# Optimization experiments

Measured on AMD Instinct MI355X. Metric: run time of the kernel, lower is better.

Reference implementation:

```python
import jax, jax.numpy as jnp
import numpy as np

EPS = 1e-6

def _conv1x1(x, w, b):
    # x: [b,c,h,w], w: [o,c], b: [o] -> per-pixel matmul
    return jnp.einsum('bchw,oc->bohw', x, w) + b[None, :, None, None]

def setup_inputs() -> dict:
    key = jax.random.key(0)
    ks = jax.random.split(key, 10)
    b, c, h, w = 16, 256, 128, 128
    dec = jax.random.normal(ks[0], (b, c, h, w), jnp.float32)
    enc = jax.random.normal(ks[1], (b, c, h, w), jnp.float32)
    ln_w = jnp.ones((c,), jnp.float32)
    ln_b = jnp.zeros((c,), jnp.float32)
    w0 = jax.random.normal(ks[2], (c, c), jnp.float32) * 0.05
    b0 = jax.random.normal(ks[3], (c,), jnp.float32) * 0.05
    w1 = jax.random.normal(ks[4], (c // 2, c), jnp.float32) * 0.05
    b1 = jax.random.normal(ks[5], (c // 2,), jnp.float32) * 0.05
    w2 = jax.random.normal(ks[6], (c // 4, c // 2), jnp.float32) * 0.05
    b2 = jax.random.normal(ks[7], (c // 4,), jnp.float32) * 0.05
    w3 = jax.random.normal(ks[8], (1, c // 4), jnp.float32) * 0.05
    b3 = jax.random.normal(ks[9], (1,), jnp.float32) * 0.05
    return dict(dec=dec, enc=enc, ln_w=ln_w, ln_b=ln_b, w0=w0, b0=b0,
                w1=w1, b1=b1, w2=w2, b2=b2, w3=w3, b3=b3)

def reference(dec, enc, ln_w, ln_b, w0, b0, w1, b1, w2, b2, w3, b3):
    b, c, h, w = dec.shape
    x = dec + enc
    # LayerNorm2d: normalize over channel dim per pixel (biased var, eps=1e-6)
    mu = jnp.mean(x, axis=1, keepdims=True)
    var = jnp.var(x, axis=1, keepdims=True)
    x = (x - mu) / jnp.sqrt(var + EPS) * ln_w[None, :, None, None] + ln_b[None, :, None, None]
    # in_conv: 1x1 conv + exact GELU
    x = jax.nn.gelu(_conv1x1(x, w0, b0), approximate=False)
    # split: local channels kept, global channels pooled and broadcast back
    local_x = x[:, :c // 2]                                   # [b,c/2,h,w]
    global_x = jnp.mean(x[:, c // 2:], axis=(2, 3), keepdims=True)  # [b,c/2,1,1]
    x = jnp.concatenate([local_x, jnp.broadcast_to(global_x, local_x.shape)], axis=1)
    # mask_pre: nc -> nc/2 -> nc/4 -> 1 with GELUs
    x = jax.nn.gelu(_conv1x1(x, w1, b1), approximate=False)
    x = jax.nn.gelu(_conv1x1(x, w2, b2), approximate=False)
    x = _conv1x1(x, w3, b3)
    return jax.nn.sigmoid(x)
```

## Files before the change

### kernel.cpp

```cpp
#include <hip/hip_runtime.h>
#include <math.h>

typedef float f32x4 __attribute__((ext_vector_type(4)));
typedef short s8v __attribute__((ext_vector_type(8)));

#define LN_EPS 1e-6f

static __device__ __forceinline__ unsigned short f2bf(float f) {
  union { float f; unsigned int u; } v; v.f = f;
  unsigned int r = (v.u + 0x7FFFu + ((v.u >> 16) & 1u)) >> 16;
  return (unsigned short)r;
}
static __device__ __forceinline__ float bf2f(unsigned short b) {
  union { float f; unsigned int u; } v; v.u = ((unsigned int)b) << 16;
  return v.f;
}
static __device__ __forceinline__ float gelu_fast(float x) {
  float t = x * x;
  float u = x * fmaf(t, 0.07135481283f, 1.5957691216f);
  float e = __expf(-u);
  return __fdividef(x, 1.0f + e);
}

__global__ void prep_kernel(const float* __restrict__ w0, const float* __restrict__ w1,
                            const float* __restrict__ w2, const float* __restrict__ lnw,
                            const float* __restrict__ lnb, const float* __restrict__ b0,
                            unsigned short* __restrict__ wt0f, unsigned short* __restrict__ w1f,
                            unsigned short* __restrict__ w2f, float* __restrict__ gacc,
                            float* __restrict__ sfold, float* __restrict__ tfold) {
  int idx = blockIdx.x * blockDim.x + threadIdx.x;
  int stride = gridDim.x * blockDim.x;
  const int N0 = 65536, N1 = 16384, N2 = 8192, N3 = 2048, N4 = 256;
  for (int i = idx; i < N0 + N1 + N2 + N3 + N4; i += stride) {
    if (i < N0) {
      int j = i & 7, l = (i >> 3) & 63, ks = (i >> 9) & 7, n0 = i >> 12;
      int k = ks * 32 + (l >> 4) * 8 + j;
      wt0f[i] = f2bf(w0[(n0 * 16 + (l & 15)) * 256 + k] * lnw[k]);
    } else if (i < N0 + N1) {
      int t = i - N0;
      int j = t & 7, l = (t >> 3) & 63, ks = (t >> 9) & 3, n0 = t >> 11;
      w1f[t] = f2bf(w1[(n0 * 16 + (l & 15)) * 256 + ks * 32 + (l >> 4) * 8 + j]);
    } else if (i < N0 + N1 + N2) {
      int t = i - N0 - N1;
      int j = t & 7, l = (t >> 3) & 63, ks = (t >> 9) & 3, n0 = t >> 11;
      w2f[t] = f2bf(w2[(n0 * 16 + (l & 15)) * 128 + ks * 32 + (l >> 4) * 8 + j]);
    } else if (i < N0 + N1 + N2 + N3) {
      gacc[i - N0 - N1 - N2] = 0.0f;
    } else {
      int n = i - N0 - N1 - N2 - N3;
      float s = 0.f, t = 0.f;
      for (int c = 0; c < 256; ++c) {
        float wv = w0[n * 256 + c];
        s += wv * lnw[c];
        t += wv * lnb[c];
      }
      sfold[n] = s;
      tfold[n] = t + b0[n];
    }
  }
}

__global__ __launch_bounds__(256, 2) void k1_kernel(
    const float* __restrict__ dec, const float* __restrict__ enc,
    const unsigned short* __restrict__ wt0f,
    const float* __restrict__ sfold, const float* __restrict__ tfold,
    unsigned short* __restrict__ yl, float* __restrict__ gacc) {
  __shared__ __align__(16) unsigned char At[64 * 512];
  __shared__ float red[16][16][8];
  __shared__ float alphaL[64], betaL[64];

  const int tid = threadIdx.x, blk = blockIdx.x;
  const int b = blk >> 8;
  const int hw0 = (blk & 255) << 6;
  const int g = tid >> 4, kq = tid & 15;
  const int lane = tid & 63, w = tid >> 6, l15 = lane & 15, lg = lane >> 4;

  f32x4 sum = {0.f, 0.f, 0.f, 0.f}, sq = {0.f, 0.f, 0.f, 0.f};
  const long base = (long)(b * 256) * 16384 + hw0 + (kq << 2);
#pragma unroll
  for (int it = 0; it < 2; ++it) {
    f32x4 xv[8];
#pragma unroll
    for (int s = 0; s < 8; ++s) {
      const int c = it * 128 + g * 8 + s;
      f32x4 d = *(const f32x4*)(dec + base + (long)c * 16384);
      f32x4 e = *(const f32x4*)(enc + base + (long)c * 16384);
      f32x4 x = d + e;
      xv[s] = x;
      sum += x;
      sq += x * x;
    }
#pragma unroll
    for (int px = 0; px < 4; ++px) {
      const int p = (kq << 2) + px;
      s8v hv;
#pragma unroll
      for (int s = 0; s < 8; ++s) hv[s] = (short)f2bf(xv[s][px]);
      const int byte = (p * 512 + it * 256 + g * 16) ^ ((p & 7) << 4);
      *(s8v*)(&At[byte]) = hv;
    }
  }

#pragma unroll
  for (int q = 0; q < 4; ++q) { red[g][kq][q] = sum[q]; red[g][kq][4 + q] = sq[q]; }
  __syncthreads();
  if (tid < 64) {
    const int kk = tid >> 2, comp = tid & 3;
    float s = 0.f, s2 = 0.f;
#pragma unroll
    for (int gg = 0; gg < 16; ++gg) { s += red[gg][kk][comp]; s2 += red[gg][kk][4 + comp]; }
    const float mu = s * (1.0f / 256.0f);
    const float var = s2 * (1.0f / 256.0f) - mu * mu;
    const float rs = rsqrtf(var + LN_EPS);
    alphaL[tid] = rs;
    betaL[tid] = -mu * rs;
  }
  __syncthreads();

  f32x4 acc[4][4];
#pragma unroll
  for (int mi = 0; mi < 4; ++mi)
#pragma unroll
    for (int ni = 0; ni < 4; ++ni) acc[mi][ni] = (f32x4){0.f, 0.f, 0.f, 0.f};

#pragma unroll
  for (int ks = 0; ks < 8; ++ks) {
    s8v a[4];
#pragma unroll
    for (int mi = 0; mi < 4; ++mi) {
      const int p = mi * 16 + l15;
      const int byte = (p * 512 + ks * 64 + lg * 16) ^ ((p & 7) << 4);
      a[mi] = *(const s8v*)(&At[byte]);
    }
#pragma unroll
    for (int ni = 0; ni < 4; ++ni) {
      const int n0 = w * 4 + ni;
      s8v bfr = *(const s8v*)(wt0f + ((n0 * 8 + ks) * 64 + lane) * 8);
#pragma unroll
      for (int mi = 0; mi < 4; ++mi)
        acc[mi][ni] = __builtin_amdgcn_mfma_f32_16x16x32_bf16(a[mi], bfr, acc[mi][ni], 0, 0, 0);
    }
  }

  float sn[4], tn[4];
#pragma unroll
  for (int ni = 0; ni < 4; ++ni) {
    const int n = w * 64 + ni * 16 + l15;
    sn[ni] = sfold[n];
    tn[ni] = tfold[n];
  }

  if (w < 2) {
#pragma unroll
    for (int mi = 0; mi < 4; ++mi) {
      const f32x4 al = *(const f32x4*)(&alphaL[mi * 16 + lg * 4]);
      const f32x4 be = *(const f32x4*)(&betaL[mi * 16 + lg * 4]);
#pragma unroll
      for (int r = 0; r < 4; ++r) {
        const int p = mi * 16 + lg * 4 + r;
        const long prow = ((long)b * 16384 + hw0 + p) * 128;
#pragma unroll
        for (int ni = 0; ni < 4; ++ni) {
          const float v = gelu_fast(fmaf(al[r], acc[mi][ni][r], fmaf(be[r], sn[ni], tn[ni])));
          yl[prow + w * 64 + ni * 16 + l15] = f2bf(v);
        }
      }
    }
  } else {
    float ps[4] = {0.f, 0.f, 0.f, 0.f};
#pragma unroll
    for (int mi = 0; mi < 4; ++mi) {
      const f32x4 al = *(const f32x4*)(&alphaL[mi * 16 + lg * 4]);
      const f32x4 be = *(const f32x4*)(&betaL[mi * 16 + lg * 4]);
#pragma unroll
      for (int r = 0; r < 4; ++r) {
#pragma unroll
        for (int ni = 0; ni < 4; ++ni)
          ps[ni] += gelu_fast(fmaf(al[r], acc[mi][ni][r], fmaf(be[r], sn[ni], tn[ni])));
      }
    }
#pragma unroll
    for (int ni = 0; ni < 4; ++ni) {
      float p2 = ps[ni];
      p2 += __shfl_xor(p2, 16, 64);
      p2 += __shfl_xor(p2, 32, 64);
      if (lane < 16) atomicAdd(&gacc[b * 128 + (w - 2) * 64 + ni * 16 + lane], p2);
    }
  }
}

__global__ void kmid_kernel(const float* __restrict__ w1, const float* __restrict__ b1,
                            const float* __restrict__ gacc, float* __restrict__ g1) {
  int b = blockIdx.x, o = threadIdx.x;
  float acc = b1[o];
  const float inv = 1.0f / 16384.0f;
  for (int c = 0; c < 128; ++c)
    acc += w1[o * 256 + 128 + c] * (gacc[b * 128 + c] * inv);
  g1[b * 128 + o] = acc;
}

__global__ __launch_bounds__(256, 4) void k2_kernel(
    const unsigned short* __restrict__ yl, const float* __restrict__ g1,
    const float* __restrict__ b2v, const float* __restrict__ w3,
    const float* __restrict__ b3, const unsigned short* __restrict__ w1f,
    const unsigned short* __restrict__ w2f, float* __restrict__ out) {
  __shared__ __align__(16) unsigned char Yt[64 * 256];
  __shared__ __align__(16) unsigned char Z1[64 * 256];
  __shared__ __align__(16) unsigned char Z2[64 * 128];
  __shared__ float part3[4][64];
  __shared__ float w3S[64];

  const int tid = threadIdx.x, blk = blockIdx.x;
  const int lane = tid & 63, w = tid >> 6, l15 = lane & 15, lg = lane >> 4;
  const int P0 = blk * 64;
  const int b = blk >> 8;

  if (tid < 64) w3S[tid] = w3[tid];

#pragma unroll
  for (int q = 0; q < 4; ++q) {
    int p = q * 16 + (tid >> 4);
    int c2 = (tid & 15) * 16;
    s8v v = *(const s8v*)((const char*)yl + (long)(P0 + p) * 256 + c2);
    int byte = (p * 256 + c2) ^ ((p & 7) << 4);
    *(s8v*)(&Yt[byte]) = v;
  }
  __syncthreads();

  f32x4 acc1[4][2];
#pragma unroll
  for (int mi = 0; mi < 4; ++mi)
#pragma unroll
    for (int ni = 0; ni < 2; ++ni) acc1[mi][ni] = (f32x4){0.f, 0.f, 0.f, 0.f};
#pragma unroll
  for (int ks = 0; ks < 4; ++ks) {
    s8v a[4];
#pragma unroll
    for (int mi = 0; mi < 4; ++mi) {
      int p = mi * 16 + l15;
      int byte = (p * 256 + ks * 64 + lg * 16) ^ ((p & 7) << 4);
      a[mi] = *(const s8v*)(&Yt[byte]);
    }
#pragma unroll
    for (int ni = 0; ni < 2; ++ni) {
      int n0 = w * 2 + ni;
      s8v bfr = *(const s8v*)(w1f + ((n0 * 4 + ks) * 64 + lane) * 8);
#pragma unroll
      for (int mi = 0; mi < 4; ++mi)
        acc1[mi][ni] = __builtin_amdgcn_mfma_f32_16x16x32_bf16(a[mi], bfr, acc1[mi][ni], 0, 0, 0);
    }
  }
#pragma unroll
  for (int ni = 0; ni < 2; ++ni) {
    int o = (w * 2 + ni) * 16 + l15;
    float bias = g1[b * 128 + o];
#pragma unroll
    for (int mi = 0; mi < 4; ++mi)
#pragma unroll
      for (int r = 0; r < 4; ++r) {
        int p = mi * 16 + lg * 4 + r;
        float v = gelu_fast(acc1[mi][ni][r] + bias);
        int byte = (p * 256 + o * 2) ^ ((p & 7) << 4);
        *(unsigned short*)(&Z1[byte]) = f2bf(v);
      }
  }
  __syncthreads();

  f32x4 acc2[4];
#pragma unroll
  for (int mi = 0; mi < 4; ++mi) acc2[mi] = (f32x4){0.f, 0.f, 0.f, 0.f};
#pragma unroll
  for (int ks = 0; ks < 4; ++ks) {
    s8v a[4];
#pragma unroll
    for (int mi = 0; mi < 4; ++mi) {
      int p = mi * 16 + l15;
      int byte = (p * 256 + ks * 64 + lg * 16) ^ ((p & 7) << 4);
      a[mi] = *(const s8v*)(&Z1[byte]);
    }
    s8v bfr = *(const s8v*)(w2f + ((w * 4 + ks) * 64 + lane) * 8);
#pragma unroll
    for (int mi = 0; mi < 4; ++mi)
      acc2[mi] = __builtin_amdgcn_mfma_f32_16x16x32_bf16(a[mi], bfr, acc2[mi], 0, 0, 0);
  }
  {
    int o = w * 16 + l15;
    float bias = b2v[o];
#pragma unroll
    for (int mi = 0; mi < 4; ++mi)
#pragma unroll
      for (int r = 0; r < 4; ++r) {
        int p = mi * 16 + lg * 4 + r;
        float v = gelu_fast(acc2[mi][r] + bias);
        int byte = (p * 128 + o * 2) ^ ((p & 7) << 4);
        *(unsigned short*)(&Z2[byte]) = f2bf(v);
      }
  }
  __syncthreads();

  {
    int p = tid & 63, cg = tid >> 6;
    float dot = 0.f;
#pragma unroll
    for (int half = 0; half < 2; ++half) {
      int byte = (p * 128 + cg * 32 + half * 16) ^ ((p & 7) << 4);
      s8v z = *(const s8v*)(&Z2[byte]);
#pragma unroll
      for (int j = 0; j < 8; ++j)
        dot += bf2f((unsigned short)z[j]) * w3S[cg * 16 + half * 8 + j];
    }
    part3[cg][p] = dot;
  }
  __syncthreads();
  if (tid < 64) {
    float t = part3[0][tid] + part3[1][tid] + part3[2][tid] + part3[3][tid] + b3[0];
    out[P0 + tid] = __fdividef(1.0f, 1.0f + __expf(-t));
  }
}

extern "C" void kernel_launch(void* const* d_in, const int* in_sizes, int n_in,
                              void* d_out, int out_size, void* d_ws, size_t ws_size,
                              hipStream_t stream) {
  const float* dec = (const float*)d_in[0];
  const float* enc = (const float*)d_in[1];
  const float* lnw = (const float*)d_in[2];
  const float* lnb = (const float*)d_in[3];
  const float* w0  = (const float*)d_in[4];
  const float* b0  = (const float*)d_in[5];
  const float* w1  = (const float*)d_in[6];
  const float* b1  = (const float*)d_in[7];
  const float* w2  = (const float*)d_in[8];
  const float* b2  = (const float*)d_in[9];
  const float* w3  = (const float*)d_in[10];
  const float* b3  = (const float*)d_in[11];

  char* ws = (char*)d_ws;
  unsigned short* yl   = (unsigned short*)ws;
  unsigned short* wt0f = (unsigned short*)(ws + 67108864);
  unsigned short* w1f  = (unsigned short*)(ws + 67239936);
  unsigned short* w2f  = (unsigned short*)(ws + 67272704);
  float* gacc          = (float*)(ws + 67289088);
  float* g1            = (float*)(ws + 67297280);
  float* sfold         = (float*)(ws + 67305472);
  float* tfold         = (float*)(ws + 67306496);

  prep_kernel<<<128, 256, 0, stream>>>(w0, w1, w2, lnw, lnb, b0, wt0f, w1f, w2f,
                                       gacc, sfold, tfold);
  k1_kernel<<<4096, 256, 0, stream>>>(dec, enc, wt0f, sfold, tfold, yl, gacc);
  kmid_kernel<<<16, 128, 0, stream>>>(w1, b1, gacc, g1);
  k2_kernel<<<4096, 256, 0, stream>>>(yl, g1, b2, w3, b3, w1f, w2f, (float*)d_out);
}
```

Baseline: 207.5 us.

## Make k1 persistent over 8 tiles with double-buffered LDS prefetch

k1 now processes eight 64-pixel tiles per block (512 blocks instead of 4096). The dec/enc loads for the next tile are issued before and during the MFMA loop on the current tile, and staged into a second LDS buffer, with LayerNorm stats computed one tile ahead. The aim is to hide global-load latency behind matrix math and cut per-block launch overhead. In exchange it doubles LDS use and raises register pressure from the prefetch arrays, which could lower occupancy. 512 blocks may also underfill the GPU.

```diff
diff --git a/kernel.cpp b/kernel.cpp
--- a/kernel.cpp
+++ b/kernel.cpp
@@ -65,44 +65,56 @@
     const unsigned short* __restrict__ wt0f,
     const float* __restrict__ sfold, const float* __restrict__ tfold,
     unsigned short* __restrict__ yl, float* __restrict__ gacc) {
-  __shared__ __align__(16) unsigned char At[64 * 512];
+  __shared__ __align__(16) unsigned char At[2][64 * 512];
   __shared__ float red[16][16][8];
-  __shared__ float alphaL[64], betaL[64];
-
-  const int tid = threadIdx.x, blk = blockIdx.x;
-  const int b = blk >> 8;
-  const int hw0 = (blk & 255) << 6;
+  __shared__ float alphaL[2][64], betaL[2][64];
+
+  const int tid = threadIdx.x;
   const int g = tid >> 4, kq = tid & 15;
   const int lane = tid & 63, w = tid >> 6, l15 = lane & 15, lg = lane >> 4;
 
-  f32x4 sum = {0.f, 0.f, 0.f, 0.f}, sq = {0.f, 0.f, 0.f, 0.f};
-  const long base = (long)(b * 256) * 16384 + hw0 + (kq << 2);
-#pragma unroll
-  for (int it = 0; it < 2; ++it) {
-    f32x4 xv[8];
-#pragma unroll
-    for (int s = 0; s < 8; ++s) {
-      const int c = it * 128 + g * 8 + s;
-      f32x4 d = *(const f32x4*)(dec + base + (long)c * 16384);
-      f32x4 e = *(const f32x4*)(enc + base + (long)c * 16384);
-      f32x4 x = d + e;
-      xv[s] = x;
-      sum += x;
-      sq += x * x;
-    }
-#pragma unroll
-    for (int px = 0; px < 4; ++px) {
-      const int p = (kq << 2) + px;
-      s8v hv;
-#pragma unroll
-      for (int s = 0; s < 8; ++s) hv[s] = (short)f2bf(xv[s][px]);
-      const int byte = (p * 512 + it * 256 + g * 16) ^ ((p & 7) << 4);
-      *(s8v*)(&At[byte]) = hv;
-    }
-  }
-
-#pragma unroll
-  for (int q = 0; q < 4; ++q) { red[g][kq][q] = sum[q]; red[g][kq][4 + q] = sq[q]; }
+  const int t0 = blockIdx.x * 8;
+  const int b = t0 >> 8;
+  const int hwb = (t0 & 255) << 6;
+  const long cbase = (long)b * 256 * 16384;
+
+  float sn[4], tn[4];
+#pragma unroll
+  for (int ni = 0; ni < 4; ++ni) {
+    const int n = w * 64 + ni * 16 + l15;
+    sn[ni] = sfold[n];
+    tn[ni] = tfold[n];
+  }
+
+  {
+    f32x4 sum = {0.f, 0.f, 0.f, 0.f}, sq = {0.f, 0.f, 0.f, 0.f};
+    const long base = cbase + hwb + (kq << 2);
+#pragma unroll
+    for (int it = 0; it < 2; ++it) {
+      f32x4 xv[8];
+#pragma unroll
+      for (int s = 0; s < 8; ++s) {
+        const int c = it * 128 + g * 8 + s;
+        f32x4 d = *(const f32x4*)(dec + base + (long)c * 16384);
+        f32x4 e = *(const f32x4*)(enc + base + (long)c * 16384);
+        f32x4 x = d + e;
+        xv[s] = x;
+        sum += x;
+        sq += x * x;
+      }
+#pragma unroll
+      for (int px = 0; px < 4; ++px) {
+        const int p = (kq << 2) + px;
+        s8v hv;
+#pragma unroll
+        for (int s = 0; s < 8; ++s) hv[s] = (short)f2bf(xv[s][px]);
+        const int byte = (p * 512 + it * 256 + g * 16) ^ ((p & 7) << 4);
+        *(s8v*)(&At[0][byte]) = hv;
+      }
+    }
+#pragma unroll
+    for (int q = 0; q < 4; ++q) { red[g][kq][q] = sum[q]; red[g][kq][4 + q] = sq[q]; }
+  }
   __syncthreads();
   if (tid < 64) {
     const int kk = tid >> 2, comp = tid & 3;
@@ -112,80 +124,172 @@
     const float mu = s * (1.0f / 256.0f);
     const float var = s2 * (1.0f / 256.0f) - mu * mu;
     const float rs = rsqrtf(var + LN_EPS);
-    alphaL[tid] = rs;
-    betaL[tid] = -mu * rs;
-  }
-  __syncthreads();
-
-  f32x4 acc[4][4];
-#pragma unroll
-  for (int mi = 0; mi < 4; ++mi)
-#pragma unroll
-    for (int ni = 0; ni < 4; ++ni) acc[mi][ni] = (f32x4){0.f, 0.f, 0.f, 0.f};
-
-#pragma unroll
-  for (int ks = 0; ks < 8; ++ks) {
-    s8v a[4];
-#pragma unroll
-    for (int mi = 0; mi < 4; ++mi) {
-      const int p = mi * 16 + l15;
-      const int byte = (p * 512 + ks * 64 + lg * 16) ^ ((p & 7) << 4);
-      a[mi] = *(const s8v*)(&At[byte]);
-    }
-#pragma unroll
-    for (int ni = 0; ni < 4; ++ni) {
-      const int n0 = w * 4 + ni;
-      s8v bfr = *(const s8v*)(wt0f + ((n0 * 8 + ks) * 64 + lane) * 8);
-#pragma unroll
-      for (int mi = 0; mi < 4; ++mi)
-        acc[mi][ni] = __builtin_amdgcn_mfma_f32_16x16x32_bf16(a[mi], bfr, acc[mi][ni], 0, 0, 0);
-    }
-  }
-
-  float sn[4], tn[4];
-#pragma unroll
-  for (int ni = 0; ni < 4; ++ni) {
-    const int n = w * 64 + ni * 16 + l15;
-    sn[ni] = sfold[n];
-    tn[ni] = tfold[n];
-  }
-
-  if (w < 2) {
-#pragma unroll
-    for (int mi = 0; mi < 4; ++mi) {
-      const f32x4 al = *(const f32x4*)(&alphaL[mi * 16 + lg * 4]);
-      const f32x4 be = *(const f32x4*)(&betaL[mi * 16 + lg * 4]);
-#pragma unroll
-      for (int r = 0; r < 4; ++r) {
-        const int p = mi * 16 + lg * 4 + r;
-        const long prow = ((long)b * 16384 + hw0 + p) * 128;
-#pragma unroll
-        for (int ni = 0; ni < 4; ++ni) {
-          const float v = gelu_fast(fmaf(al[r], acc[mi][ni][r], fmaf(be[r], sn[ni], tn[ni])));
-          yl[prow + w * 64 + ni * 16 + l15] = f2bf(v);
+    alphaL[0][tid] = rs;
+    betaL[0][tid] = -mu * rs;
+  }
+  __syncthreads();
+
+  for (int i = 0; i < 8; ++i) {
+    const int cur = i & 1, nxt = cur ^ 1;
+    const bool hasnext = (i < 7);
+    const int hw0 = hwb + i * 64;
+    const long nb = cbase + hw0 + 64 + (kq << 2);
+
+    f32x4 dv[8], ev[8];
+    f32x4 sum = {0.f, 0.f, 0.f, 0.f}, sq = {0.f, 0.f, 0.f, 0.f};
+
+    if (hasnext) {
+#pragma unroll
+      for (int s = 0; s < 8; ++s) {
+        const int c = g * 8 + s;
+        dv[s] = *(const f32x4*)(dec + nb + (long)c * 16384);
+        ev[s] = *(const f32x4*)(enc + nb + (long)c * 16384);
+      }
+    }
+
+    f32x4 acc[4][4];
+#pragma unroll
+    for (int mi = 0; mi < 4; ++mi)
+#pragma unroll
+      for (int ni = 0; ni < 4; ++ni) acc[mi][ni] = (f32x4){0.f, 0.f, 0.f, 0.f};
+
+#pragma unroll
+    for (int ks = 0; ks < 4; ++ks) {
+      s8v a[4];
+#pragma unroll
+      for (int mi = 0; mi < 4; ++mi) {
+        const int p = mi * 16 + l15;
+        const int byte = (p * 512 + ks * 64 + lg * 16) ^ ((p & 7) << 4);
+        a[mi] = *(const s8v*)(&At[cur][byte]);
+      }
+#pragma unroll
+      for (int ni = 0; ni < 4; ++ni) {
+        const int n0 = w * 4 + ni;
+        s8v bfr = *(const s8v*)(wt0f + ((n0 * 8 + ks) * 64 + lane) * 8);
+#pragma unroll
+        for (int mi = 0; mi < 4; ++mi)
+          acc[mi][ni] = __builtin_amdgcn_mfma_f32_16x16x32_bf16(a[mi], bfr, acc[mi][ni], 0, 0, 0);
+      }
+    }
+
+    if (hasnext) {
+      f32x4 xv[8];
+#pragma unroll
+      for (int s = 0; s < 8; ++s) {
+        f32x4 x = dv[s] + ev[s];
+        xv[s] = x;
+        sum += x;
+        sq += x * x;
+      }
+#pragma unroll
+      for (int s = 0; s < 8; ++s) {
+        const int c = 128 + g * 8 + s;
+        dv[s] = *(const f32x4*)(dec + nb + (long)c * 16384);
+        ev[s] = *(const f32x4*)(enc + nb + (long)c * 16384);
+      }
+#pragma unroll
+      for (int px = 0; px < 4; ++px) {
+        const int p = (kq << 2) + px;
+        s8v hv;
+#pragma unroll
+        for (int s = 0; s < 8; ++s) hv[s] = (short)f2bf(xv[s][px]);
+        const int byte = (p * 512 + g * 16) ^ ((p & 7) << 4);
+        *(s8v*)(&At[nxt][byte]) = hv;
+      }
+    }
+
+#pragma unroll
+    for (int ks = 4; ks < 8; ++ks) {
+      s8v a[4];
+#pragma unroll
+      for (int mi = 0; mi < 4; ++mi) {
+        const int p = mi * 16 + l15;
+        const int byte = (p * 512 + ks * 64 + lg * 16) ^ ((p & 7) << 4);
+        a[mi] = *(const s8v*)(&At[cur][byte]);
+      }
+#pragma unroll
+      for (int ni = 0; ni < 4; ++ni) {
+        const int n0 = w * 4 + ni;
+        s8v bfr = *(const s8v*)(wt0f + ((n0 * 8 + ks) * 64 + lane) * 8);
+#pragma unroll
+        for (int mi = 0; mi < 4; ++mi)
+          acc[mi][ni] = __builtin_amdgcn_mfma_f32_16x16x32_bf16(a[mi], bfr, acc[mi][ni], 0, 0, 0);
+      }
+    }
+
+    if (hasnext) {
+      f32x4 xv[8];
+#pragma unroll
+      for (int s = 0; s < 8; ++s) {
+        f32x4 x = dv[s] + ev[s];
+        xv[s] = x;
+        sum += x;
+        sq += x * x;
+      }
+#pragma unroll
+      for (int px = 0; px < 4; ++px) {
+        const int p = (kq << 2) + px;
+        s8v hv;
+#pragma unroll
+        for (int s = 0; s < 8; ++s) hv[s] = (short)f2bf(xv[s][px]);
+        const int byte = (p * 512 + 256 + g * 16) ^ ((p & 7) << 4);
+        *(s8v*)(&At[nxt][byte]) = hv;
+      }
+#pragma unroll
+      for (int q = 0; q < 4; ++q) { red[g][kq][q] = sum[q]; red[g][kq][4 + q] = sq[q]; }
+    }
+
+    if (w < 2) {
+#pragma unroll
+      for (int mi = 0; mi < 4; ++mi) {
+        const f32x4 al = *(const f32x4*)(&alphaL[cur][mi * 16 + lg * 4]);
+        const f32x4 be = *(const f32x4*)(&betaL[cur][mi * 16 + lg * 4]);
+#pragma unroll
+        for (int r = 0; r < 4; ++r) {
+          const int p = mi * 16 + lg * 4 + r;
+          const long prow = ((long)b * 16384 + hw0 + p) * 128;
+#pragma unroll
+          for (int ni = 0; ni < 4; ++ni) {
+            const float v = gelu_fast(fmaf(al[r], acc[mi][ni][r], fmaf(be[r], sn[ni], tn[ni])));
+            yl[prow + w * 64 + ni * 16 + l15] = f2bf(v);
+          }
         }
       }
-    }
-  } else {
-    float ps[4] = {0.f, 0.f, 0.f, 0.f};
-#pragma unroll
-    for (int mi = 0; mi < 4; ++mi) {
-      const f32x4 al = *(const f32x4*)(&alphaL[mi * 16 + lg * 4]);
-      const f32x4 be = *(const f32x4*)(&betaL[mi * 16 + lg * 4]);
-#pragma unroll
-      for (int r = 0; r < 4; ++r) {
-#pragma unroll
-        for (int ni = 0; ni < 4; ++ni)
-          ps[ni] += gelu_fast(fmaf(al[r], acc[mi][ni][r], fmaf(be[r], sn[ni], tn[ni])));
-      }
-    }
-#pragma unroll
-    for (int ni = 0; ni < 4; ++ni) {
-      float p2 = ps[ni];
-      p2 += __shfl_xor(p2, 16, 64);
-      p2 += __shfl_xor(p2, 32, 64);
-      if (lane < 16) atomicAdd(&gacc[b * 128 + (w - 2) * 64 + ni * 16 + lane], p2);
-    }
+    } else {
+      float ps[4] = {0.f, 0.f, 0.f, 0.f};
+#pragma unroll
+      for (int mi = 0; mi < 4; ++mi) {
+        const f32x4 al = *(const f32x4*)(&alphaL[cur][mi * 16 + lg * 4]);
+        const f32x4 be = *(const f32x4*)(&betaL[cur][mi * 16 + lg * 4]);
+#pragma unroll
+        for (int r = 0; r < 4; ++r) {
+#pragma unroll
+          for (int ni = 0; ni < 4; ++ni)
+            ps[ni] += gelu_fast(fmaf(al[r], acc[mi][ni][r], fmaf(be[r], sn[ni], tn[ni])));
+        }
+      }
+#pragma unroll
+      for (int ni = 0; ni < 4; ++ni) {
+        float p2 = ps[ni];
+        p2 += __shfl_xor(p2, 16, 64);
+        p2 += __shfl_xor(p2, 32, 64);
+        if (lane < 16) atomicAdd(&gacc[b * 128 + (w - 2) * 64 + ni * 16 + lane], p2);
+      }
+    }
+
+    __syncthreads();
+    if (hasnext && tid < 64) {
+      const int kk = tid >> 2, comp = tid & 3;
+      float s = 0.f, s2 = 0.f;
+#pragma unroll
+      for (int gg = 0; gg < 16; ++gg) { s += red[gg][kk][comp]; s2 += red[gg][kk][4 + comp]; }
+      const float mu = s * (1.0f / 256.0f);
+      const float var = s2 * (1.0f / 256.0f) - mu * mu;
+      const float rs = rsqrtf(var + LN_EPS);
+      alphaL[nxt][tid] = rs;
+      betaL[nxt][tid] = -mu * rs;
+    }
+    __syncthreads();
   }
 }
 
@@ -346,7 +450,7 @@
 
   prep_kernel<<<128, 256, 0, stream>>>(w0, w1, w2, lnw, lnb, b0, wt0f, w1f, w2f,
                                        gacc, sfold, tfold);
-  k1_kernel<<<4096, 256, 0, stream>>>(dec, enc, wt0f, sfold, tfold, yl, gacc);
+  k1_kernel<<<512, 256, 0, stream>>>(dec, enc, wt0f, sfold, tfold, yl, gacc);
   kmid_kernel<<<16, 128, 0, stream>>>(w1, b1, gacc, g1);
   k2_kernel<<<4096, 256, 0, stream>>>(yl, g1, b2, w3, b3, w1f, w2f, (float*)d_out);
 }
```

Measured after the change: 524.6 us. 153% more time.
